# Optimization experiments

Hardware: AMD Instinct MI355X
Metric: run time of the kernel (lower is better)

Reference implementation:

```python
import jax, jax.numpy as jnp
import numpy as np

B, T, IN, H = 32, 256, 64, 128
TOP_K = 5
TRUNC = 100   # truncate_length: detach h,c every TRUNC steps
EPS = 1e-7
NEG = -1e9


def setup_inputs() -> dict:
    key = jax.random.key(0)
    ks = jax.random.split(key, 6)
    s = 1.0 / np.sqrt(H)  # torch LSTMCell default init bound
    xav = float(1.414 * np.sqrt(6.0 / (2 * H + 1)))  # xavier_uniform gain=1.414
    return {
        "x": jax.random.normal(ks[0], (B, T, IN), jnp.float32),
        "W_ih": jax.random.uniform(ks[1], (4 * H, IN), jnp.float32, -s, s),
        "W_hh": jax.random.uniform(ks[2], (4 * H, H), jnp.float32, -s, s),
        "b_ih": jax.random.uniform(ks[3], (4 * H,), jnp.float32, -s, s),
        "b_hh": jax.random.uniform(ks[4], (4 * H,), jnp.float32, -s, s),
        "w_t": jax.random.uniform(ks[5], (2 * H, 1), jnp.float32, -xav, xav),
    }


def _lstm_cell(x_t, h, c, W_ih, W_hh, b_ih, b_hh):
    # torch gate order: i, f, g, o
    g = x_t @ W_ih.T + h @ W_hh.T + (b_ih + b_hh)
    i, f, gg, o = jnp.split(g, 4, axis=-1)
    c = jax.nn.sigmoid(f) * c + jax.nn.sigmoid(i) * jnp.tanh(gg)
    h = jax.nn.sigmoid(o) * jnp.tanh(c)
    return h, c


def reference(x, W_ih, W_hh, b_ih, b_hh, w_t):
    Bv, Tv, _ = x.shape
    Hh = W_hh.shape[1]
    # score = w_t . tanh(cat(h_t, h_old)) splits additively since tanh is elementwise
    w_a = w_t[:Hh, 0]
    w_b = w_t[Hh:, 0]
    pos = jnp.arange(Tv + 1)

    def step(carry, inp):
        h, c, h_old = carry          # h_old: [B, T+1, H], slot 0 = initial zeros
        i, x_t = inp
        det = ((i + 1) % TRUNC) == 0
        h = jnp.where(det, jax.lax.stop_gradient(h), h)
        c = jnp.where(det, jax.lax.stop_gradient(c), c)
        h, c = _lstm_cell(x_t, h, c, W_ih, W_hh, b_ih, b_hh)
        rem = i + 1                  # remember_size
        mask = pos < rem             # [T+1] valid memory slots
        # attention scores over stored states
        s = (jnp.tanh(h) @ w_a)[:, None] + jnp.tanh(h_old) @ w_b  # [B, T+1]
        s_valid = jnp.where(mask[None, :], s, NEG)
        delta = jax.lax.top_k(s_valid, TOP_K)[0][:, -1] + EPS
        w_sp = jnp.clip(s_valid - delta[:, None], 0.0)
        w_sp = w_sp / (w_sp.sum(axis=1, keepdims=True) + EPS)
        # Sparse_attention returns raw scores when remember_size <= top_k
        attn_w = jnp.where(rem <= TOP_K, s, w_sp)
        attn_c = jnp.einsum('bt,bth->bh', jnp.where(mask[None, :], attn_w, 0.0), h_old)
        h = h + attn_c
        h_old = jax.lax.dynamic_update_slice(h_old, h[:, None, :], (0, rem, 0))
        return (h, c, h_old), (attn_c, attn_w)

    h0 = jnp.zeros((Bv, Hh), x.dtype)
    c0 = jnp.zeros((Bv, Hh), x.dtype)
    buf0 = jnp.zeros((Bv, Tv + 1, Hh), x.dtype)
    xs = (jnp.arange(Tv), jnp.swapaxes(x, 0, 1))
    _, (attn_c_all, attn_w_all) = jax.lax.scan(step, (h0, c0, buf0), xs)
    # module returns last step's (attn_c, out_attn_w); final remember_size == T
    return attn_c_all[-1], attn_w_all[-1][:, :Tv, None]
```

## Files before the change

kernel.cpp:

```cpp
#include <hip/hip_runtime.h>
#include <math.h>

#define NEGF -1000000000.0f
#define EPSF 1e-7f


__device__ __forceinline__ float fsigmoid(float x) {
  return 1.0f / (1.0f + __expf(-x));
}
__device__ __forceinline__ float ftanh(float x) {
  return 1.0f - 2.0f / (1.0f + __expf(2.0f * x));
}

__device__ __forceinline__ float wave_allsum(float v) {
#if __has_builtin(__builtin_amdgcn_update_dpp) && __has_builtin(__builtin_amdgcn_readlane)
  float f = v;
#define DPPSTEP(ctrl, rmask) { \
    int t = __builtin_amdgcn_update_dpp(0, __builtin_bit_cast(int, f), \
                                        ctrl, rmask, 0xf, true); \
    f += __builtin_bit_cast(float, t); }
  DPPSTEP(0x111, 0xf)
  DPPSTEP(0x112, 0xf)
  DPPSTEP(0x114, 0xf)
  DPPSTEP(0x118, 0xf)
  DPPSTEP(0x142, 0xa)
  DPPSTEP(0x143, 0x8)
#undef DPPSTEP
  return __builtin_bit_cast(float,
      __builtin_amdgcn_readlane(__builtin_bit_cast(int, f), 63));
#else
  for (int off = 1; off < 64; off <<= 1) v += __shfl_xor(v, off, 64);
  return v;
#endif
}

__global__ __launch_bounds__(256) void xw_kernel(
    const float* __restrict__ x, const float* __restrict__ W_ih,
    const float* __restrict__ b_ih, const float* __restrict__ b_hh,
    float* __restrict__ xw)
{
  const int t0 = blockIdx.x * 8;
  const int b  = blockIdx.y;
  const int g  = (blockIdx.z << 8) + threadIdx.x;

  __shared__ float sx[8][64];
  {
    const float* src = x + (size_t)(b * 256 + t0) * 64;
    ((float2*)&sx[0][0])[threadIdx.x] = ((const float2*)src)[threadIdx.x];
  }
  const float4* wr = (const float4*)(W_ih + (size_t)g * 64);
  float4 w0 = wr[0],  w1 = wr[1],  w2 = wr[2],  w3 = wr[3],
         w4 = wr[4],  w5 = wr[5],  w6 = wr[6],  w7 = wr[7],
         w8 = wr[8],  w9 = wr[9],  w10 = wr[10], w11 = wr[11],
         w12 = wr[12], w13 = wr[13], w14 = wr[14], w15 = wr[15];
  const float bias = b_ih[g] + b_hh[g];
  __syncthreads();
  for (int tt = 0; tt < 8; ++tt) {
    const float4* sx4 = (const float4*)(&sx[tt][0]);
    float a0 = 0.0f, a1 = 0.0f, a2 = 0.0f, a3 = 0.0f;
#define XSTEP(j) { float4 hv = sx4[j]; \
    a0 = fmaf(w##j.x, hv.x, a0); a1 = fmaf(w##j.y, hv.y, a1); \
    a2 = fmaf(w##j.z, hv.z, a2); a3 = fmaf(w##j.w, hv.w, a3); }
    XSTEP(0) XSTEP(1) XSTEP(2) XSTEP(3) XSTEP(4) XSTEP(5) XSTEP(6) XSTEP(7)
    XSTEP(8) XSTEP(9) XSTEP(10) XSTEP(11) XSTEP(12) XSTEP(13) XSTEP(14) XSTEP(15)
#undef XSTEP
    xw[(size_t)(b * 256 + t0 + tt) * 512 + g] = (a0 + a1) + (a2 + a3) + bias;
  }
}

__global__
__attribute__((amdgpu_flat_work_group_size(1024, 1024), amdgpu_waves_per_eu(4, 4)))
void lstm_attn(
    const float* __restrict__ xw, const float* __restrict__ W_hh,
    const float* __restrict__ w_t, float* __restrict__ out)
{
  const int b   = blockIdx.x;
  const int tid = threadIdx.x;
  const int l   = tid & 63;
  const int wid = tid >> 6;
  const int p   = tid & 255;
  const int q   = tid >> 8;
  const int gA  = p;
  const int gB  = p + 256;

  __shared__ float ho[257 * 128];
  __shared__ float sh_part[4 * 512];
  __shared__ float sh_d[8];

  const float4* pA = (const float4*)(W_hh + (size_t)gA * 128 + (q << 5));
  const float4* pB = (const float4*)(W_hh + (size_t)gB * 128 + (q << 5));
  float4 wA0 = pA[0], wA1 = pA[1], wA2 = pA[2], wA3 = pA[3],
         wA4 = pA[4], wA5 = pA[5], wA6 = pA[6], wA7 = pA[7];
  float4 wB0 = pB[0], wB1 = pB[1], wB2 = pB[2], wB3 = pB[3],
         wB4 = pB[4], wB5 = pB[5], wB6 = pB[6], wB7 = pB[7];

  const int j0 = 2 * l, j1 = 2 * l + 1;
  float c0 = 0.0f, c1 = 0.0f;
  float wa0 = 0.0f, wa1 = 0.0f, wb0 = 0.0f, wb1 = 0.0f;
  float t5v0 = 0.0f, t5v1 = NEGF, t5v2 = NEGF, t5v3 = NEGF, t5v4 = NEGF;
  int   t5i0 = 0, t5i1 = 0, t5i2 = 0, t5i3 = 0;
  float gn0 = 0.0f, gn1 = 0.0f, gn2 = 0.0f, gn3 = 0.0f;
  int   ofs0 = 0, ofs1 = 0, ofs2 = 0, ofs3 = 0;

  if (wid == 0) {
    wa0 = w_t[j0];       wa1 = w_t[j1];
    wb0 = w_t[128 + j0]; wb1 = w_t[128 + j1];
    *(float2*)(ho + j0) = make_float2(0.0f, 0.0f);
    __builtin_amdgcn_s_setprio(1);
  }
  if (tid == 0) sh_d[0] = 0.0f;
  __syncthreads();

  const float* xwb = xw + (size_t)b * 256 * 512;
  float xcurA = 0.0f, xcurB = 0.0f;
  if (q == 0) { xcurA = xwb[gA]; xcurB = xwb[gB]; }

  for (int i = 0; i < 256; ++i) {
    const int rem = i + 1;
    float hn0 = 0.0f, hn1 = 0.0f;

    float aA0 = xcurA, aA1 = 0.0f, aB0 = xcurB, aB1 = 0.0f;
    if (q == 0 && i < 255) {
      xcurA = xwb[(size_t)(i + 1) * 512 + gA];
      xcurB = xwb[(size_t)(i + 1) * 512 + gB];
    }
    const float4* hh4 = (const float4*)(ho + i * 128 + (q << 5));
#define LSTEP(j) { float4 hv = hh4[j]; \
    aA0 = fmaf(wA##j.x, hv.x, aA0); aA1 = fmaf(wA##j.y, hv.y, aA1); \
    aA0 = fmaf(wA##j.z, hv.z, aA0); aA1 = fmaf(wA##j.w, hv.w, aA1); \
    aB0 = fmaf(wB##j.x, hv.x, aB0); aB1 = fmaf(wB##j.y, hv.y, aB1); \
    aB0 = fmaf(wB##j.z, hv.z, aB0); aB1 = fmaf(wB##j.w, hv.w, aB1); }
    LSTEP(0) LSTEP(1) LSTEP(2) LSTEP(3) LSTEP(4) LSTEP(5) LSTEP(6) LSTEP(7)
#undef LSTEP
    sh_part[(q << 9) + gA] = aA0 + aA1;
    sh_part[(q << 9) + gB] = aB0 + aB1;

    float2 hv0, hv1, hv2, hv3;
    if (wid == 0 && i >= 5) {
      hv0 = *(const float2*)(ho + ofs0);
      hv1 = *(const float2*)(ho + ofs1);
      hv2 = *(const float2*)(ho + ofs2);
      hv3 = *(const float2*)(ho + ofs3);
    }
    __syncthreads();

    if (wid == 0) {
#define GSUM(base) ({ \
      float2 x0 = ((const float2*)(sh_part        + (base)))[l]; \
      float2 x1 = ((const float2*)(sh_part +  512 + (base)))[l]; \
      float2 x2 = ((const float2*)(sh_part + 1024 + (base)))[l]; \
      float2 x3 = ((const float2*)(sh_part + 1536 + (base)))[l]; \
      float2 r; r.x = (x0.x + x1.x) + (x2.x + x3.x); \
      r.y = (x0.y + x1.y) + (x2.y + x3.y); r; })
      float2 Pi = GSUM(0), Pf = GSUM(128), Pg = GSUM(256), Po = GSUM(384);
#undef GSUM
      c0 = fsigmoid(Pf.x) * c0 + fsigmoid(Pi.x) * ftanh(Pg.x);
      c1 = fsigmoid(Pf.y) * c1 + fsigmoid(Pi.y) * ftanh(Pg.y);
      float hc0 = fsigmoid(Po.x) * ftanh(c0);
      float hc1 = fsigmoid(Po.y) * ftanh(c1);

      float at0, at1;
      if (i >= 5) {
        at0 = gn0 * hv0.x;            at1 = gn0 * hv0.y;
        at0 = fmaf(gn1, hv1.x, at0);  at1 = fmaf(gn1, hv1.y, at1);
        at0 = fmaf(gn2, hv2.x, at0);  at1 = fmaf(gn2, hv2.y, at1);
        at0 = fmaf(gn3, hv3.x, at0);  at1 = fmaf(gn3, hv3.y, at1);
      } else {
        float a = wave_allsum(ftanh(hc0) * wa0 + ftanh(hc1) * wa1);
        at0 = 0.0f; at1 = 0.0f;
        for (int t = 0; t <= i; ++t) {
          float s = a + sh_d[t];
          float2 hv = *(const float2*)(ho + t * 128 + j0);
          at0 = fmaf(s, hv.x, at0);
          at1 = fmaf(s, hv.y, at1);
        }
      }
      hn0 = hc0 + at0; hn1 = hc1 + at1;
      *(float2*)(ho + rem * 128 + j0) = make_float2(hn0, hn1);
      if (i == 255) {
        out[b * 128 + j0] = at0; out[b * 128 + j1] = at1;
        #pragma unroll
        for (int m = 0; m < 4; ++m) {
          int t = l + 64 * m;
          float val = 0.0f;
          if (t == t5i0) val = gn0;
          if (t == t5i1) val = gn1;
          if (t == t5i2) val = gn2;
          if (t == t5i3) val = gn3;
          out[4096 + b * 256 + t] = val;
        }
      }
    }
    __syncthreads();

    if (wid == 0 && i < 255) {
      float dn = wave_allsum(ftanh(hn0) * wb0 + ftanh(hn1) * wb1);
      if (l == 0 && i < 4) sh_d[rem] = dn;
      float v = dn; int vi = rem;
      if (v > t5v0) { float tv = t5v0; int ti = t5i0; t5v0 = v; t5i0 = vi; v = tv; vi = ti; }
      if (v > t5v1) { float tv = t5v1; int ti = t5i1; t5v1 = v; t5i1 = vi; v = tv; vi = ti; }
      if (v > t5v2) { float tv = t5v2; int ti = t5i2; t5v2 = v; t5i2 = vi; v = tv; vi = ti; }
      if (v > t5v3) { float tv = t5v3; int ti = t5i3; t5v3 = v; t5i3 = vi; v = tv; vi = ti; }
      if (v > t5v4) { t5v4 = v; }
      float g0 = fmaxf(t5v0 - t5v4 - EPSF, 0.0f);
      float g1 = fmaxf(t5v1 - t5v4 - EPSF, 0.0f);
      float g2 = fmaxf(t5v2 - t5v4 - EPSF, 0.0f);
      float g3 = fmaxf(t5v3 - t5v4 - EPSF, 0.0f);
      float inv = 1.0f / (((g0 + g1) + (g2 + g3)) + EPSF);
      gn0 = g0 * inv; gn1 = g1 * inv; gn2 = g2 * inv; gn3 = g3 * inv;
      ofs0 = (t5i0 << 7) + j0; ofs1 = (t5i1 << 7) + j0;
      ofs2 = (t5i2 << 7) + j0; ofs3 = (t5i3 << 7) + j0;
    }
  }
}

extern "C" void kernel_launch(void* const* d_in, const int* in_sizes, int n_in,
                              void* d_out, int out_size, void* d_ws, size_t ws_size,
                              hipStream_t stream) {
  const float* x    = (const float*)d_in[0];
  const float* W_ih = (const float*)d_in[1];
  const float* W_hh = (const float*)d_in[2];
  const float* b_ih = (const float*)d_in[3];
  const float* b_hh = (const float*)d_in[4];
  const float* w_t  = (const float*)d_in[5];
  float* out = (float*)d_out;

  float* xw = (float*)d_ws;

  xw_kernel<<<dim3(32, 32, 2), 256, 0, stream>>>(x, W_ih, b_ih, b_hh, xw);
  lstm_attn<<<dim3(32), 1024, 0, stream>>>(xw, W_hh, w_t, out);
}
```

Before: 414.6 us.

## Fuse input projection into recurrent LSTM kernel and vectorize gate FMAs

Removes the separate kernel that precomputed x@W_ih plus biases into a large workspace. Each thread now keeps its W_ih row slice in registers and computes the input projection per step from an x row staged into a double-buffered shared array by one wave. This drops one kernel launch and the global write and read of the projected gates. The cost is extra register pressure and extra FMAs inside the serial loop. Gate accumulation also switches to 4-wide vector FMAs with four partial sums.

```diff
diff --git a/kernel.cpp b/kernel.cpp
--- a/kernel.cpp
+++ b/kernel.cpp
@@ -4,6 +4,9 @@
 #define NEGF -1000000000.0f
 #define EPSF 1e-7f
 
+
+typedef float v4f __attribute__((ext_vector_type(4)));
+#define FMA4(a, b, c) __builtin_elementwise_fma((a), (b), (c))
 
 __device__ __forceinline__ float fsigmoid(float x) {
   return 1.0f / (1.0f + __expf(-x));
@@ -34,45 +37,13 @@
 #endif
 }
 
-__global__ __launch_bounds__(256) void xw_kernel(
-    const float* __restrict__ x, const float* __restrict__ W_ih,
-    const float* __restrict__ b_ih, const float* __restrict__ b_hh,
-    float* __restrict__ xw)
-{
-  const int t0 = blockIdx.x * 8;
-  const int b  = blockIdx.y;
-  const int g  = (blockIdx.z << 8) + threadIdx.x;
-
-  __shared__ float sx[8][64];
-  {
-    const float* src = x + (size_t)(b * 256 + t0) * 64;
-    ((float2*)&sx[0][0])[threadIdx.x] = ((const float2*)src)[threadIdx.x];
-  }
-  const float4* wr = (const float4*)(W_ih + (size_t)g * 64);
-  float4 w0 = wr[0],  w1 = wr[1],  w2 = wr[2],  w3 = wr[3],
-         w4 = wr[4],  w5 = wr[5],  w6 = wr[6],  w7 = wr[7],
-         w8 = wr[8],  w9 = wr[9],  w10 = wr[10], w11 = wr[11],
-         w12 = wr[12], w13 = wr[13], w14 = wr[14], w15 = wr[15];
-  const float bias = b_ih[g] + b_hh[g];
-  __syncthreads();
-  for (int tt = 0; tt < 8; ++tt) {
-    const float4* sx4 = (const float4*)(&sx[tt][0]);
-    float a0 = 0.0f, a1 = 0.0f, a2 = 0.0f, a3 = 0.0f;
-#define XSTEP(j) { float4 hv = sx4[j]; \
-    a0 = fmaf(w##j.x, hv.x, a0); a1 = fmaf(w##j.y, hv.y, a1); \
-    a2 = fmaf(w##j.z, hv.z, a2); a3 = fmaf(w##j.w, hv.w, a3); }
-    XSTEP(0) XSTEP(1) XSTEP(2) XSTEP(3) XSTEP(4) XSTEP(5) XSTEP(6) XSTEP(7)
-    XSTEP(8) XSTEP(9) XSTEP(10) XSTEP(11) XSTEP(12) XSTEP(13) XSTEP(14) XSTEP(15)
-#undef XSTEP
-    xw[(size_t)(b * 256 + t0 + tt) * 512 + g] = (a0 + a1) + (a2 + a3) + bias;
-  }
-}
-
 __global__
 __attribute__((amdgpu_flat_work_group_size(1024, 1024), amdgpu_waves_per_eu(4, 4)))
 void lstm_attn(
-    const float* __restrict__ xw, const float* __restrict__ W_hh,
-    const float* __restrict__ w_t, float* __restrict__ out)
+    const float* __restrict__ x, const float* __restrict__ W_ih,
+    const float* __restrict__ W_hh, const float* __restrict__ b_ih,
+    const float* __restrict__ b_hh, const float* __restrict__ w_t,
+    float* __restrict__ out)
 {
   const int b   = blockIdx.x;
   const int tid = threadIdx.x;
@@ -85,14 +56,21 @@
 
   __shared__ float ho[257 * 128];
   __shared__ float sh_part[4 * 512];
+  __shared__ float sx[2][64];
   __shared__ float sh_d[8];
 
-  const float4* pA = (const float4*)(W_hh + (size_t)gA * 128 + (q << 5));
-  const float4* pB = (const float4*)(W_hh + (size_t)gB * 128 + (q << 5));
-  float4 wA0 = pA[0], wA1 = pA[1], wA2 = pA[2], wA3 = pA[3],
-         wA4 = pA[4], wA5 = pA[5], wA6 = pA[6], wA7 = pA[7];
-  float4 wB0 = pB[0], wB1 = pB[1], wB2 = pB[2], wB3 = pB[3],
-         wB4 = pB[4], wB5 = pB[5], wB6 = pB[6], wB7 = pB[7];
+  const v4f* pA = (const v4f*)(W_hh + (size_t)gA * 128 + (q << 5));
+  const v4f* pB = (const v4f*)(W_hh + (size_t)gB * 128 + (q << 5));
+  v4f wA0 = pA[0], wA1 = pA[1], wA2 = pA[2], wA3 = pA[3],
+      wA4 = pA[4], wA5 = pA[5], wA6 = pA[6], wA7 = pA[7];
+  v4f wB0 = pB[0], wB1 = pB[1], wB2 = pB[2], wB3 = pB[3],
+      wB4 = pB[4], wB5 = pB[5], wB6 = pB[6], wB7 = pB[7];
+  const v4f* iAp = (const v4f*)(W_ih + (size_t)gA * 64 + (q << 4));
+  const v4f* iBp = (const v4f*)(W_ih + (size_t)gB * 64 + (q << 4));
+  v4f iA0 = iAp[0], iA1 = iAp[1], iA2 = iAp[2], iA3 = iAp[3];
+  v4f iB0 = iBp[0], iB1 = iBp[1], iB2 = iBp[2], iB3 = iBp[3];
+  float biasA = 0.0f, biasB = 0.0f;
+  if (q == 0) { biasA = b_ih[gA] + b_hh[gA]; biasB = b_ih[gB] + b_hh[gB]; }
 
   const int j0 = 2 * l, j1 = 2 * l + 1;
   float c0 = 0.0f, c1 = 0.0f;
@@ -102,38 +80,40 @@
   float gn0 = 0.0f, gn1 = 0.0f, gn2 = 0.0f, gn3 = 0.0f;
   int   ofs0 = 0, ofs1 = 0, ofs2 = 0, ofs3 = 0;
 
+  const float* xg = x + (size_t)b * 256 * 64;
+
   if (wid == 0) {
     wa0 = w_t[j0];       wa1 = w_t[j1];
     wb0 = w_t[128 + j0]; wb1 = w_t[128 + j1];
     *(float2*)(ho + j0) = make_float2(0.0f, 0.0f);
     __builtin_amdgcn_s_setprio(1);
   }
+  if (wid == 15) sx[0][l] = xg[l];
   if (tid == 0) sh_d[0] = 0.0f;
   __syncthreads();
-
-  const float* xwb = xw + (size_t)b * 256 * 512;
-  float xcurA = 0.0f, xcurB = 0.0f;
-  if (q == 0) { xcurA = xwb[gA]; xcurB = xwb[gB]; }
 
   for (int i = 0; i < 256; ++i) {
     const int rem = i + 1;
     float hn0 = 0.0f, hn1 = 0.0f;
 
-    float aA0 = xcurA, aA1 = 0.0f, aB0 = xcurB, aB1 = 0.0f;
-    if (q == 0 && i < 255) {
-      xcurA = xwb[(size_t)(i + 1) * 512 + gA];
-      xcurB = xwb[(size_t)(i + 1) * 512 + gB];
-    }
-    const float4* hh4 = (const float4*)(ho + i * 128 + (q << 5));
-#define LSTEP(j) { float4 hv = hh4[j]; \
-    aA0 = fmaf(wA##j.x, hv.x, aA0); aA1 = fmaf(wA##j.y, hv.y, aA1); \
-    aA0 = fmaf(wA##j.z, hv.z, aA0); aA1 = fmaf(wA##j.w, hv.w, aA1); \
-    aB0 = fmaf(wB##j.x, hv.x, aB0); aB1 = fmaf(wB##j.y, hv.y, aB1); \
-    aB0 = fmaf(wB##j.z, hv.z, aB0); aB1 = fmaf(wB##j.w, hv.w, aB1); }
+    float xnext = 0.0f;
+    if (wid == 15 && i < 255) xnext = xg[(size_t)(i + 1) * 64 + l];
+
+    const v4f* xr = (const v4f*)(&sx[i & 1][q << 4]);
+    v4f xv0 = xr[0], xv1 = xr[1], xv2 = xr[2], xv3 = xr[3];
+    v4f accA = {biasA, 0.0f, 0.0f, 0.0f};
+    v4f accB = {biasB, 0.0f, 0.0f, 0.0f};
+    accA = FMA4(iA0, xv0, accA); accA = FMA4(iA1, xv1, accA);
+    accA = FMA4(iA2, xv2, accA); accA = FMA4(iA3, xv3, accA);
+    accB = FMA4(iB0, xv0, accB); accB = FMA4(iB1, xv1, accB);
+    accB = FMA4(iB2, xv2, accB); accB = FMA4(iB3, xv3, accB);
+    const v4f* hh4 = (const v4f*)(ho + i * 128 + (q << 5));
+#define LSTEP(j) { v4f hv = hh4[j]; \
+    accA = FMA4(wA##j, hv, accA); accB = FMA4(wB##j, hv, accB); }
     LSTEP(0) LSTEP(1) LSTEP(2) LSTEP(3) LSTEP(4) LSTEP(5) LSTEP(6) LSTEP(7)
 #undef LSTEP
-    sh_part[(q << 9) + gA] = aA0 + aA1;
-    sh_part[(q << 9) + gB] = aB0 + aB1;
+    sh_part[(q << 9) + gA] = (accA.x + accA.y) + (accA.z + accA.w);
+    sh_part[(q << 9) + gB] = (accB.x + accB.y) + (accB.z + accB.w);
 
     float2 hv0, hv1, hv2, hv3;
     if (wid == 0 && i >= 5) {
@@ -190,6 +170,8 @@
           out[4096 + b * 256 + t] = val;
         }
       }
+    } else if (wid == 15 && i < 255) {
+      sx[(i + 1) & 1][l] = xnext;
     }
     __syncthreads();
 
@@ -225,8 +207,6 @@
   const float* w_t  = (const float*)d_in[5];
   float* out = (float*)d_out;
 
-  float* xw = (float*)d_ws;
-
-  xw_kernel<<<dim3(32, 32, 2), 256, 0, stream>>>(x, W_ih, b_ih, b_hh, xw);
-  lstm_attn<<<dim3(32), 1024, 0, stream>>>(xw, W_hh, w_t, out);
-}
+  (void)d_ws; (void)ws_size;
+  lstm_attn<<<dim3(32), 1024, 0, stream>>>(x, W_ih, W_hh, b_ih, b_hh, w_t, out);
+}
```

Result: slower. 1.006 ms (+142.6%).
